# Performance work log

Measured on AMD Instinct MI355X. Metric: run time of the kernel, lower is better.

## Reference

```python
import jax, jax.numpy as jnp
import numpy as np

LAMBDA = 0.7
K = 3
HIDDEN = 8
IN_F = 512
OUT_F = 256
N = 4096


def _gat_layer(x, adj, W, a):
    # h = fc(x); e[i,j] = attn([h_i ; h_j]) = h_i @ a[:F] + h_j @ a[F:]
    # (same math as the N*N repeat/cat/linear, without materializing [N*N, 2F])
    h = x @ W                      # [N, F]
    F_ = h.shape[1]
    src = h @ a[:F_]               # [N, 1]
    dst = h @ a[F_:]               # [N, 1]
    e = src + dst.T                # [N, N]
    att = jax.nn.softmax(e, axis=1) * adj
    return jax.nn.elu(att @ h)     # [N, F]


def setup_inputs() -> dict:
    key = jax.random.key(0)
    ks = jax.random.split(key, 8)
    x = jax.random.normal(ks[0], (N, IN_F), dtype=jnp.float32)
    # binarized sparse-ish adjacency stored densely (avg degree ~41)
    adj = (jax.random.uniform(ks[1], (N, N)) < 0.01).astype(jnp.float32)
    W1 = jax.random.normal(ks[2], (IN_F, HIDDEN), dtype=jnp.float32) * (1.0 / np.sqrt(IN_F))
    a1 = jax.random.normal(ks[3], (2 * HIDDEN, 1), dtype=jnp.float32) * (1.0 / np.sqrt(2 * HIDDEN))
    W2 = jax.random.normal(ks[4], (HIDDEN, 1), dtype=jnp.float32) * (1.0 / np.sqrt(HIDDEN))
    a2 = jax.random.normal(ks[5], (2, 1), dtype=jnp.float32)
    W_sgc = jax.random.normal(ks[6], (IN_F * K, OUT_F), dtype=jnp.float32) * (1.0 / np.sqrt(IN_F * K))
    b_sgc = jnp.zeros((OUT_F,), dtype=jnp.float32)
    return {"x": x, "adj": adj, "W1": W1, "a1": a1, "W2": W2, "a2": a2,
            "W_sgc": W_sgc, "b_sgc": b_sgc}


def reference(x, adj, W1, a1, W2, a2, W_sgc, b_sgc):
    # GAT scoring head (dropout p=0.6 is identity at inference)
    h1 = _gat_layer(x, adj, W1, a1)
    node_scores = _gat_layer(h1, adj, W2, a2)        # [N, 1]

    # K-hop adjacency powers
    adj_list = [adj]
    for _ in range(1, K):
        adj_list.append(adj_list[-1] @ adj)

    # dynamic per-row masking (row-broadcast of node_scores > lambda)
    change_mask = (node_scores > LAMBDA).astype(adj.dtype)  # [N, 1] broadcasts over cols
    for k in range(K - 1):
        adj_list[k] = adj_list[k] * change_mask
        adj_list[k + 1] = adj_list[k + 1] * (1.0 - change_mask)

    # SGC: concat K hop-aggregated features, then linear
    agg = jnp.concatenate([A @ x for A in adj_list], axis=1)  # [N, K*IN_F]
    return agg @ W_sgc + b_sgc
```

## Files before the change

kernel.cpp:

```cpp
#include <hip/hip_runtime.h>
#include <hip/hip_bf16.h>
#include <cstddef>

#define NNODE 4096
#define INF   512
#define OUTF  256
#define HID   8
#define CAP   128

typedef __attribute__((ext_vector_type(8))) short short8;
typedef __attribute__((ext_vector_type(4))) float f32x4;
typedef __attribute__((ext_vector_type(2))) float f32x2;

__device__ __forceinline__ unsigned short f2bf(float f){
  unsigned int u = __float_as_uint(f);
  u += 0x7fffu + ((u >> 16) & 1u);
  return (unsigned short)(u >> 16);
}

__global__ __launch_bounds__(256) void build_csr(const float* __restrict__ adj,
                                                 int* __restrict__ deg,
                                                 int* __restrict__ cols){
  int row = blockIdx.x, tid = threadIdx.x;
  __shared__ int cnt;
  if (tid == 0) cnt = 0;
  __syncthreads();
  const float4* arow = (const float4*)(adj + (size_t)row * NNODE);
  int* crow = cols + (size_t)row * CAP;
  #pragma unroll
  for (int k = 0; k < 4; k++){
    int idx = k * 256 + tid;
    float4 v = arow[idx];
    int n0 = (v.x != 0.f), n1 = (v.y != 0.f), n2 = (v.z != 0.f), n3 = (v.w != 0.f);
    int m = n0 + n1 + n2 + n3;
    if (m){
      int base = atomicAdd(&cnt, m);
      int c = idx * 4;
      if (n0){ if (base < CAP) crow[base] = c;     base++; }
      if (n1){ if (base < CAP) crow[base] = c + 1; base++; }
      if (n2){ if (base < CAP) crow[base] = c + 2; base++; }
      if (n3){ if (base < CAP) crow[base] = c + 3; }
    }
  }
  __syncthreads();
  if (tid == 0) deg[row] = cnt > CAP ? CAP : cnt;
}

__global__ __launch_bounds__(256) void gat_h(const float* __restrict__ x,
                                             const float* __restrict__ W1,
                                             const float* __restrict__ a1,
                                             float* __restrict__ h,
                                             float* __restrict__ dstv,
                                             unsigned short* __restrict__ xb){
  int wave = threadIdx.x >> 6, lane = threadIdx.x & 63;
  int row = blockIdx.x * 4 + wave;
  const float* xr = x + (size_t)row * INF;
  unsigned short* xbr = xb + (size_t)row * INF;
  float acc[HID];
  #pragma unroll
  for (int f = 0; f < HID; f++) acc[f] = 0.f;
  for (int k = lane; k < INF; k += 64){
    float xv = xr[k];
    xbr[k] = f2bf(xv);
    const float* wp = W1 + (size_t)k * HID;
    #pragma unroll
    for (int f = 0; f < HID; f++) acc[f] += xv * wp[f];
  }
  #pragma unroll
  for (int f = 0; f < HID; f++)
    for (int o = 32; o >= 1; o >>= 1) acc[f] += __shfl_xor(acc[f], o, 64);
  if (lane == 0){
    float d = 0.f;
    #pragma unroll
    for (int f = 0; f < HID; f++){ h[(size_t)row*HID + f] = acc[f]; d += acc[f] * a1[HID + f]; }
    dstv[row] = d;
  }
}

__global__ __launch_bounds__(1024) void softmax_p(const float* __restrict__ dstv,
                                                  float* __restrict__ p){
  __shared__ float red[16];
  int tid = threadIdx.x, lane = tid & 63, wv = tid >> 6;
  float mx = -INFINITY;
  for (int i = tid; i < NNODE; i += 1024) mx = fmaxf(mx, dstv[i]);
  #pragma unroll
  for (int o = 32; o >= 1; o >>= 1) mx = fmaxf(mx, __shfl_xor(mx, o, 64));
  if (lane == 0) red[wv] = mx;
  __syncthreads();
  mx = red[0];
  #pragma unroll
  for (int k = 1; k < 16; k++) mx = fmaxf(mx, red[k]);
  __syncthreads();
  float sum = 0.f;
  for (int i = tid; i < NNODE; i += 1024){ float e = expf(dstv[i] - mx); p[i] = e; sum += e; }
  #pragma unroll
  for (int o = 32; o >= 1; o >>= 1) sum += __shfl_xor(sum, o, 64);
  if (lane == 0) red[wv] = sum;
  __syncthreads();
  float tot = 0.f;
  #pragma unroll
  for (int k = 0; k < 16; k++) tot += red[k];
  float inv = 1.0f / tot;
  for (int i = tid; i < NNODE; i += 1024) p[i] *= inv;
}

__global__ __launch_bounds__(256) void gat_agg1(const float* __restrict__ h,
                                                const float* __restrict__ p,
                                                const int* __restrict__ deg,
                                                const int* __restrict__ cols,
                                                const float* __restrict__ W2,
                                                float* __restrict__ h2){
  int wave = threadIdx.x >> 6, lane = threadIdx.x & 63;
  int row = blockIdx.x * 4 + wave;
  const int* cl = cols + (size_t)row * CAP;
  int d = deg[row];
  int ng = lane >> 3;
  int f  = lane & 7;
  float acc = 0.f;
  for (int n = ng; n < d; n += 8){
    int j = cl[n];
    acc += p[j] * h[(size_t)j * HID + f];
  }
  acc += __shfl_xor(acc, 8, 64);
  acc += __shfl_xor(acc, 16, 64);
  acc += __shfl_xor(acc, 32, 64);
  float e = acc > 0.f ? acc : expm1f(acc);
  float t = e * W2[f];
  t += __shfl_xor(t, 1, 64);
  t += __shfl_xor(t, 2, 64);
  t += __shfl_xor(t, 4, 64);
  if (lane == 0) h2[row] = t;
}

__global__ __launch_bounds__(1024) void softmax_q(const float* __restrict__ h2,
                                                  const float* __restrict__ a2,
                                                  float* __restrict__ q){
  __shared__ float red[16];
  int tid = threadIdx.x, lane = tid & 63, wv = tid >> 6;
  float s2 = a2[1];
  float mx = -INFINITY;
  for (int i = tid; i < NNODE; i += 1024) mx = fmaxf(mx, s2 * h2[i]);
  #pragma unroll
  for (int o = 32; o >= 1; o >>= 1) mx = fmaxf(mx, __shfl_xor(mx, o, 64));
  if (lane == 0) red[wv] = mx;
  __syncthreads();
  mx = red[0];
  #pragma unroll
  for (int k = 1; k < 16; k++) mx = fmaxf(mx, red[k]);
  __syncthreads();
  float sum = 0.f;
  for (int i = tid; i < NNODE; i += 1024){ float e = expf(s2 * h2[i] - mx); q[i] = e; sum += e; }
  #pragma unroll
  for (int o = 32; o >= 1; o >>= 1) sum += __shfl_xor(sum, o, 64);
  if (lane == 0) red[wv] = sum;
  __syncthreads();
  float tot = 0.f;
  #pragma unroll
  for (int k = 0; k < 16; k++) tot += red[k];
  float inv = 1.0f / tot;
  for (int i = tid; i < NNODE; i += 1024) q[i] = q[i] * inv * h2[i];
}

__global__ __launch_bounds__(256) void scores_mask(const float* __restrict__ q,
                                                   const int* __restrict__ deg,
                                                   const int* __restrict__ cols,
                                                   float* __restrict__ maskf){
  int wave = threadIdx.x >> 6, lane = threadIdx.x & 63;
  int row = blockIdx.x * 4 + wave;
  const int* cl = cols + (size_t)row * CAP;
  int d = deg[row];
  float s = 0.f;
  for (int n = lane; n < d; n += 64) s += q[cl[n]];
  #pragma unroll
  for (int o = 32; o >= 1; o >>= 1) s += __shfl_xor(s, o, 64);
  if (lane == 0){
    float e = s > 0.f ? s : expm1f(s);
    maskf[row] = (e > 0.7f) ? 1.0f : 0.0f;
  }
}

__global__ void convert_w(const float* __restrict__ Wsgc, unsigned short* __restrict__ wbT){
  int idx = blockIdx.x * 256 + threadIdx.x;
  if (idx >= 512 * 512) return;
  int c = idx >> 9, k = idx & 511;
  float val = (c < 256) ? Wsgc[(size_t)k * OUTF + c]
                        : Wsgc[(size_t)(1024 + k) * OUTF + (c - 256)];
  wbT[idx] = f2bf(val);
}

__global__ __launch_bounds__(256) void gemm_xw(const unsigned short* __restrict__ XB,
                                               const unsigned short* __restrict__ BT,
                                               float* __restrict__ G){
  __shared__ unsigned short As[64][72];
  __shared__ unsigned short Bs[64][72];
  int tid = threadIdx.x;
  int wave = tid >> 6, lane = tid & 63;
  int row0 = blockIdx.x * 64;
  int col0 = blockIdx.y * 64;
  int wr = wave >> 1, wc = wave & 1;
  f32x4 acc[2][2];
  #pragma unroll
  for (int i = 0; i < 2; i++)
    #pragma unroll
    for (int j = 0; j < 2; j++)
      #pragma unroll
      for (int e = 0; e < 4; e++) acc[i][j][e] = 0.f;

  int mrow = lane & 15;
  int kq = (lane >> 4) * 8;

  for (int k0 = 0; k0 < 512; k0 += 64){
    #pragma unroll
    for (int ps = 0; ps < 2; ps++){
      int idx = ps * 256 + tid;
      int r = idx >> 3;
      int ko = (idx & 7) * 8;
      *(int4*)(&As[r][ko]) = *(const int4*)(XB + ((size_t)(row0 + r) * 512 + k0 + ko));
      *(int4*)(&Bs[r][ko]) = *(const int4*)(BT + ((size_t)(col0 + r) * 512 + k0 + ko));
    }
    __syncthreads();
    #pragma unroll
    for (int kk = 0; kk < 2; kk++){
      short8 a[2], b[2];
      #pragma unroll
      for (int i = 0; i < 2; i++)
        a[i] = *(const short8*)(&As[wr * 32 + i * 16 + mrow][kk * 32 + kq]);
      #pragma unroll
      for (int j = 0; j < 2; j++)
        b[j] = *(const short8*)(&Bs[wc * 32 + j * 16 + mrow][kk * 32 + kq]);
      #pragma unroll
      for (int i = 0; i < 2; i++)
        #pragma unroll
        for (int j = 0; j < 2; j++)
          acc[i][j] = __builtin_amdgcn_mfma_f32_16x16x32_bf16(a[i], b[j], acc[i][j], 0, 0, 0);
    }
    __syncthreads();
  }
  int crow = (lane >> 4) * 4;
  int ccol = lane & 15;
  #pragma unroll
  for (int i = 0; i < 2; i++)
    #pragma unroll
    for (int j = 0; j < 2; j++)
      #pragma unroll
      for (int e = 0; e < 4; e++){
        int r = row0 + wr * 32 + i * 16 + crow + e;
        int c = col0 + wc * 32 + j * 16 + ccol;
        G[(size_t)r * 512 + c] = acc[i][j][e];
      }
}

__global__ __launch_bounds__(256) void hop_half(const float* __restrict__ in, int instride,
                                                int colbase,
                                                float* __restrict__ out,
                                                const int* __restrict__ deg,
                                                const int* __restrict__ cols){
  int wave = threadIdx.x >> 6, lane = threadIdx.x & 63;
  int row = blockIdx.x * 4 + wave;
  const int* cl = cols + (size_t)row * CAP;
  int d = deg[row];
  const float* src = in + colbase;
  f32x2 acc = {0.f, 0.f};
  f32x2 acc2 = {0.f, 0.f};
  int n = 0;
  for (; n + 8 <= d; n += 8){
    int j0 = cl[n],   j1 = cl[n+1], j2 = cl[n+2], j3 = cl[n+3];
    int j4 = cl[n+4], j5 = cl[n+5], j6 = cl[n+6], j7 = cl[n+7];
    f32x2 a = ((const f32x2*)(src + (size_t)j0 * instride))[lane];
    f32x2 b = ((const f32x2*)(src + (size_t)j1 * instride))[lane];
    f32x2 c = ((const f32x2*)(src + (size_t)j2 * instride))[lane];
    f32x2 e = ((const f32x2*)(src + (size_t)j3 * instride))[lane];
    f32x2 f = ((const f32x2*)(src + (size_t)j4 * instride))[lane];
    f32x2 g = ((const f32x2*)(src + (size_t)j5 * instride))[lane];
    f32x2 hh = ((const f32x2*)(src + (size_t)j6 * instride))[lane];
    f32x2 ii = ((const f32x2*)(src + (size_t)j7 * instride))[lane];
    acc  += a + b + c + e;
    acc2 += f + g + hh + ii;
  }
  for (; n < d; n++)
    acc += ((const f32x2*)(src + (size_t)cl[n] * instride))[lane];
  ((f32x2*)(out + (size_t)row * OUTF + colbase))[lane] = acc + acc2;
}

__global__ __launch_bounds__(256) void hop_final_half(const float* __restrict__ Gleft,
                                                      const float* __restrict__ T2,
                                                      const float* __restrict__ maskf,
                                                      const float* __restrict__ b,
                                                      int colbase,
                                                      float* __restrict__ out,
                                                      const int* __restrict__ deg,
                                                      const int* __restrict__ cols){
  int wave = threadIdx.x >> 6, lane = threadIdx.x & 63;
  int row = blockIdx.x * 4 + wave;
  const int* cl = cols + (size_t)row * CAP;
  int d = deg[row];
  bool m = maskf[row] != 0.0f;
  const float* src = (m ? Gleft : T2) + colbase;
  int instride    = m ? 512   : 256;
  f32x2 acc = {0.f, 0.f};
  f32x2 acc2 = {0.f, 0.f};
  int n = 0;
  for (; n + 8 <= d; n += 8){
    int j0 = cl[n],   j1 = cl[n+1], j2 = cl[n+2], j3 = cl[n+3];
    int j4 = cl[n+4], j5 = cl[n+5], j6 = cl[n+6], j7 = cl[n+7];
    f32x2 a = ((const f32x2*)(src + (size_t)j0 * instride))[lane];
    f32x2 bb = ((const f32x2*)(src + (size_t)j1 * instride))[lane];
    f32x2 c = ((const f32x2*)(src + (size_t)j2 * instride))[lane];
    f32x2 e = ((const f32x2*)(src + (size_t)j3 * instride))[lane];
    f32x2 f = ((const f32x2*)(src + (size_t)j4 * instride))[lane];
    f32x2 g = ((const f32x2*)(src + (size_t)j5 * instride))[lane];
    f32x2 hh = ((const f32x2*)(src + (size_t)j6 * instride))[lane];
    f32x2 ii = ((const f32x2*)(src + (size_t)j7 * instride))[lane];
    acc  += a + bb + c + e;
    acc2 += f + g + hh + ii;
  }
  for (; n < d; n++)
    acc += ((const f32x2*)(src + (size_t)cl[n] * instride))[lane];
  f32x2 bias = ((const f32x2*)(b + colbase))[lane];
  ((f32x2*)(out + (size_t)row * OUTF + colbase))[lane] = acc + acc2 + bias;
}

extern "C" void kernel_launch(void* const* d_in, const int* in_sizes, int n_in,
                              void* d_out, int out_size, void* d_ws, size_t ws_size,
                              hipStream_t stream) {
  const float* x    = (const float*)d_in[0];
  const float* adj  = (const float*)d_in[1];
  const float* W1   = (const float*)d_in[2];
  const float* a1   = (const float*)d_in[3];
  const float* W2   = (const float*)d_in[4];
  const float* a2   = (const float*)d_in[5];
  const float* Wsgc = (const float*)d_in[6];
  const float* bsgc = (const float*)d_in[7];
  float* out = (float*)d_out;

  char* w = (char*)d_ws;
  size_t off = 0;
  auto carve = [&](size_t bytes) -> char* {
    char* p = w + off;
    off += (bytes + 255) & ~(size_t)255;
    return p;
  };
  int*   deg   = (int*)carve((size_t)NNODE * 4);
  int*   cols  = (int*)carve((size_t)NNODE * CAP * 4);
  float* h     = (float*)carve((size_t)NNODE * HID * 4);
  float* dstv  = (float*)carve((size_t)NNODE * 4);
  float* p     = (float*)carve((size_t)NNODE * 4);
  float* h2    = (float*)carve((size_t)NNODE * 4);
  float* q     = (float*)carve((size_t)NNODE * 4);
  float* maskf = (float*)carve((size_t)NNODE * 4);
  unsigned short* wbT = (unsigned short*)carve((size_t)512 * 512 * 2);
  unsigned short* xb  = (unsigned short*)carve((size_t)NNODE * INF * 2);
  float* G  = (float*)carve((size_t)NNODE * 512 * 4);
  float* T1 = (float*)carve((size_t)NNODE * OUTF * 4);
  float* T2 = (float*)carve((size_t)NNODE * OUTF * 4);

  build_csr<<<NNODE, 256, 0, stream>>>(adj, deg, cols);

  gat_h<<<NNODE / 4, 256, 0, stream>>>(x, W1, a1, h, dstv, xb);
  softmax_p<<<1, 1024, 0, stream>>>(dstv, p);
  gat_agg1<<<NNODE / 4, 256, 0, stream>>>(h, p, deg, cols, W2, h2);
  softmax_q<<<1, 1024, 0, stream>>>(h2, a2, q);
  scores_mask<<<NNODE / 4, 256, 0, stream>>>(q, deg, cols, maskf);

  convert_w<<<1024, 256, 0, stream>>>(Wsgc, wbT);
  dim3 gg(64, 8);
  gemm_xw<<<gg, 256, 0, stream>>>(xb, wbT, G);

  hop_half<<<NNODE / 4, 256, 0, stream>>>(G + 256, 512, 0,   T1, deg, cols);
  hop_half<<<NNODE / 4, 256, 0, stream>>>(G + 256, 512, 128, T1, deg, cols);
  hop_half<<<NNODE / 4, 256, 0, stream>>>(T1, 256, 0,   T2, deg, cols);
  hop_half<<<NNODE / 4, 256, 0, stream>>>(T1, 256, 128, T2, deg, cols);
  hop_final_half<<<NNODE / 4, 256, 0, stream>>>(G, T2, maskf, bsgc, 0,   out, deg, cols);
  hop_final_half<<<NNODE / 4, 256, 0, stream>>>(G, T2, maskf, bsgc, 128, out, deg, cols);
}
```

Before: 205.6 us.

## Store hop intermediates in bf16, pad CSR rows, merge hop halves, enlarge GEMM tile

The GEMM output G and the hop buffers T1/T2 are now stored as bf16 instead of fp32, which halves the bytes moved by the sparse gather kernels. CSR rows are padded to a multiple of 8 with a sentinel index that points at a zeroed extra row, so the tail handling is simpler. Each hop now runs as one kernel where half-waves gather 8 bf16 values per lane and combine with a shuffle, and the GEMM tile grows from 64x64 to 128x128. The cost is extra rounding error from bf16 intermediates and higher register pressure in the GEMM.

```diff
diff --git a/kernel.cpp b/kernel.cpp
--- a/kernel.cpp
+++ b/kernel.cpp
@@ -10,12 +10,14 @@
 
 typedef __attribute__((ext_vector_type(8))) short short8;
 typedef __attribute__((ext_vector_type(4))) float f32x4;
-typedef __attribute__((ext_vector_type(2))) float f32x2;
 
 __device__ __forceinline__ unsigned short f2bf(float f){
   unsigned int u = __float_as_uint(f);
   u += 0x7fffu + ((u >> 16) & 1u);
   return (unsigned short)(u >> 16);
+}
+__device__ __forceinline__ float bf2f(unsigned short s){
+  return __uint_as_float((unsigned int)s << 16);
 }
 
 __global__ __launch_bounds__(256) void build_csr(const float* __restrict__ adj,
@@ -43,7 +45,11 @@
     }
   }
   __syncthreads();
-  if (tid == 0) deg[row] = cnt > CAP ? CAP : cnt;
+  int c = cnt > CAP ? CAP : cnt;
+  int c8 = (c + 7) & ~7;
+  if (c8 > CAP) c8 = CAP;
+  if (tid < c8 - c) crow[c + tid] = NNODE;
+  if (tid == 0) deg[row] = c8;
 }
 
 __global__ __launch_bounds__(256) void gat_h(const float* __restrict__ x,
@@ -52,6 +58,8 @@
                                              float* __restrict__ h,
                                              float* __restrict__ dstv,
                                              unsigned short* __restrict__ xb){
+  if (blockIdx.x == 0 && threadIdx.x < HID)
+    h[(size_t)NNODE * HID + threadIdx.x] = 0.f;
   int wave = threadIdx.x >> 6, lane = threadIdx.x & 63;
   int row = blockIdx.x * 4 + wave;
   const float* xr = x + (size_t)row * INF;
@@ -81,6 +89,7 @@
                                                   float* __restrict__ p){
   __shared__ float red[16];
   int tid = threadIdx.x, lane = tid & 63, wv = tid >> 6;
+  if (tid == 0) p[NNODE] = 0.f;
   float mx = -INFINITY;
   for (int i = tid; i < NNODE; i += 1024) mx = fmaxf(mx, dstv[i]);
   #pragma unroll
@@ -137,6 +146,7 @@
                                                   float* __restrict__ q){
   __shared__ float red[16];
   int tid = threadIdx.x, lane = tid & 63, wv = tid >> 6;
+  if (tid == 0) q[NNODE] = 0.f;
   float s2 = a2[1];
   float mx = -INFINITY;
   for (int i = tid; i < NNODE; i += 1024) mx = fmaxf(mx, s2 * h2[i]);
@@ -179,8 +189,13 @@
   }
 }
 
-__global__ void convert_w(const float* __restrict__ Wsgc, unsigned short* __restrict__ wbT){
+__global__ void convert_w(const float* __restrict__ Wsgc, unsigned short* __restrict__ wbT,
+                          unsigned short* __restrict__ Gb,
+                          unsigned short* __restrict__ T1,
+                          unsigned short* __restrict__ T2){
   int idx = blockIdx.x * 256 + threadIdx.x;
+  if (idx < 512) Gb[(size_t)NNODE * 512 + idx] = 0;
+  if (idx < 256){ T1[(size_t)NNODE * 256 + idx] = 0; T2[(size_t)NNODE * 256 + idx] = 0; }
   if (idx >= 512 * 512) return;
   int c = idx >> 9, k = idx & 511;
   float val = (c < 256) ? Wsgc[(size_t)k * OUTF + c]
@@ -190,19 +205,19 @@
 
 __global__ __launch_bounds__(256) void gemm_xw(const unsigned short* __restrict__ XB,
                                                const unsigned short* __restrict__ BT,
-                                               float* __restrict__ G){
-  __shared__ unsigned short As[64][72];
-  __shared__ unsigned short Bs[64][72];
+                                               unsigned short* __restrict__ Gb){
+  __shared__ unsigned short As[128][72];
+  __shared__ unsigned short Bs[128][72];
   int tid = threadIdx.x;
   int wave = tid >> 6, lane = tid & 63;
-  int row0 = blockIdx.x * 64;
-  int col0 = blockIdx.y * 64;
+  int row0 = blockIdx.x * 128;
+  int col0 = blockIdx.y * 128;
   int wr = wave >> 1, wc = wave & 1;
-  f32x4 acc[2][2];
-  #pragma unroll
-  for (int i = 0; i < 2; i++)
-    #pragma unroll
-    for (int j = 0; j < 2; j++)
+  f32x4 acc[4][4];
+  #pragma unroll
+  for (int i = 0; i < 4; i++)
+    #pragma unroll
+    for (int j = 0; j < 4; j++)
       #pragma unroll
       for (int e = 0; e < 4; e++) acc[i][j][e] = 0.f;
 
@@ -211,7 +226,7 @@
 
   for (int k0 = 0; k0 < 512; k0 += 64){
     #pragma unroll
-    for (int ps = 0; ps < 2; ps++){
+    for (int ps = 0; ps < 4; ps++){
       int idx = ps * 256 + tid;
       int r = idx >> 3;
       int ko = (idx & 7) * 8;
@@ -221,17 +236,17 @@
     __syncthreads();
     #pragma unroll
     for (int kk = 0; kk < 2; kk++){
-      short8 a[2], b[2];
+      short8 a[4], b[4];
       #pragma unroll
-      for (int i = 0; i < 2; i++)
-        a[i] = *(const short8*)(&As[wr * 32 + i * 16 + mrow][kk * 32 + kq]);
+      for (int i = 0; i < 4; i++)
+        a[i] = *(const short8*)(&As[wr * 64 + i * 16 + mrow][kk * 32 + kq]);
       #pragma unroll
-      for (int j = 0; j < 2; j++)
-        b[j] = *(const short8*)(&Bs[wc * 32 + j * 16 + mrow][kk * 32 + kq]);
+      for (int j = 0; j < 4; j++)
+        b[j] = *(const short8*)(&Bs[wc * 64 + j * 16 + mrow][kk * 32 + kq]);
       #pragma unroll
-      for (int i = 0; i < 2; i++)
+      for (int i = 0; i < 4; i++)
         #pragma unroll
-        for (int j = 0; j < 2; j++)
+        for (int j = 0; j < 4; j++)
           acc[i][j] = __builtin_amdgcn_mfma_f32_16x16x32_bf16(a[i], b[j], acc[i][j], 0, 0, 0);
     }
     __syncthreads();
@@ -239,85 +254,136 @@
   int crow = (lane >> 4) * 4;
   int ccol = lane & 15;
   #pragma unroll
-  for (int i = 0; i < 2; i++)
-    #pragma unroll
-    for (int j = 0; j < 2; j++)
+  for (int i = 0; i < 4; i++)
+    #pragma unroll
+    for (int j = 0; j < 4; j++)
       #pragma unroll
       for (int e = 0; e < 4; e++){
-        int r = row0 + wr * 32 + i * 16 + crow + e;
-        int c = col0 + wc * 32 + j * 16 + ccol;
-        G[(size_t)r * 512 + c] = acc[i][j][e];
+        int r = row0 + wr * 64 + i * 16 + crow + e;
+        int c = col0 + wc * 64 + j * 16 + ccol;
+        Gb[(size_t)r * 512 + c] = f2bf(acc[i][j][e]);
       }
 }
 
-__global__ __launch_bounds__(256) void hop_half(const float* __restrict__ in, int instride,
-                                                int colbase,
-                                                float* __restrict__ out,
-                                                const int* __restrict__ deg,
-                                                const int* __restrict__ cols){
+__global__ __launch_bounds__(256) void hop_bf(const unsigned short* __restrict__ in, int instride,
+                                              int colbase,
+                                              unsigned short* __restrict__ out,
+                                              const int* __restrict__ deg,
+                                              const int* __restrict__ cols){
   int wave = threadIdx.x >> 6, lane = threadIdx.x & 63;
   int row = blockIdx.x * 4 + wave;
   const int* cl = cols + (size_t)row * CAP;
   int d = deg[row];
-  const float* src = in + colbase;
-  f32x2 acc = {0.f, 0.f};
-  f32x2 acc2 = {0.f, 0.f};
+  int half = lane >> 5, cid = lane & 31;
+  const unsigned short* src = in + colbase + cid * 8;
+  float acc[8];
+  #pragma unroll
+  for (int e = 0; e < 8; e++) acc[e] = 0.f;
   int n = 0;
-  for (; n + 8 <= d; n += 8){
-    int j0 = cl[n],   j1 = cl[n+1], j2 = cl[n+2], j3 = cl[n+3];
-    int j4 = cl[n+4], j5 = cl[n+5], j6 = cl[n+6], j7 = cl[n+7];
-    f32x2 a = ((const f32x2*)(src + (size_t)j0 * instride))[lane];
-    f32x2 b = ((const f32x2*)(src + (size_t)j1 * instride))[lane];
-    f32x2 c = ((const f32x2*)(src + (size_t)j2 * instride))[lane];
-    f32x2 e = ((const f32x2*)(src + (size_t)j3 * instride))[lane];
-    f32x2 f = ((const f32x2*)(src + (size_t)j4 * instride))[lane];
-    f32x2 g = ((const f32x2*)(src + (size_t)j5 * instride))[lane];
-    f32x2 hh = ((const f32x2*)(src + (size_t)j6 * instride))[lane];
-    f32x2 ii = ((const f32x2*)(src + (size_t)j7 * instride))[lane];
-    acc  += a + b + c + e;
-    acc2 += f + g + hh + ii;
-  }
-  for (; n < d; n++)
-    acc += ((const f32x2*)(src + (size_t)cl[n] * instride))[lane];
-  ((f32x2*)(out + (size_t)row * OUTF + colbase))[lane] = acc + acc2;
-}
-
-__global__ __launch_bounds__(256) void hop_final_half(const float* __restrict__ Gleft,
-                                                      const float* __restrict__ T2,
-                                                      const float* __restrict__ maskf,
-                                                      const float* __restrict__ b,
-                                                      int colbase,
-                                                      float* __restrict__ out,
-                                                      const int* __restrict__ deg,
-                                                      const int* __restrict__ cols){
+  for (; n + 16 <= d; n += 16){
+    int j0 = cl[n +      half], j1 = cl[n + 2  + half], j2 = cl[n + 4  + half], j3 = cl[n + 6  + half];
+    int j4 = cl[n + 8  + half], j5 = cl[n + 10 + half], j6 = cl[n + 12 + half], j7 = cl[n + 14 + half];
+    short8 v0 = *(const short8*)(src + (size_t)j0 * instride);
+    short8 v1 = *(const short8*)(src + (size_t)j1 * instride);
+    short8 v2 = *(const short8*)(src + (size_t)j2 * instride);
+    short8 v3 = *(const short8*)(src + (size_t)j3 * instride);
+    short8 v4 = *(const short8*)(src + (size_t)j4 * instride);
+    short8 v5 = *(const short8*)(src + (size_t)j5 * instride);
+    short8 v6 = *(const short8*)(src + (size_t)j6 * instride);
+    short8 v7 = *(const short8*)(src + (size_t)j7 * instride);
+    #pragma unroll
+    for (int e = 0; e < 8; e++){
+      acc[e] += bf2f((unsigned short)v0[e]) + bf2f((unsigned short)v1[e])
+              + bf2f((unsigned short)v2[e]) + bf2f((unsigned short)v3[e])
+              + bf2f((unsigned short)v4[e]) + bf2f((unsigned short)v5[e])
+              + bf2f((unsigned short)v6[e]) + bf2f((unsigned short)v7[e]);
+    }
+  }
+  if (n < d){
+    int j0 = cl[n + half], j1 = cl[n + 2 + half], j2 = cl[n + 4 + half], j3 = cl[n + 6 + half];
+    short8 v0 = *(const short8*)(src + (size_t)j0 * instride);
+    short8 v1 = *(const short8*)(src + (size_t)j1 * instride);
+    short8 v2 = *(const short8*)(src + (size_t)j2 * instride);
+    short8 v3 = *(const short8*)(src + (size_t)j3 * instride);
+    #pragma unroll
+    for (int e = 0; e < 8; e++){
+      acc[e] += bf2f((unsigned short)v0[e]) + bf2f((unsigned short)v1[e])
+              + bf2f((unsigned short)v2[e]) + bf2f((unsigned short)v3[e]);
+    }
+  }
+  #pragma unroll
+  for (int e = 0; e < 8; e++) acc[e] += __shfl_xor(acc[e], 32, 64);
+  if (half == 0){
+    union { short8 v; unsigned short u[8]; } pk;
+    #pragma unroll
+    for (int e = 0; e < 8; e++) pk.u[e] = f2bf(acc[e]);
+    *(short8*)(out + (size_t)row * OUTF + cid * 8) = pk.v;
+  }
+}
+
+__global__ __launch_bounds__(256) void hop_final_bf(const unsigned short* __restrict__ Gb,
+                                                    const unsigned short* __restrict__ T2,
+                                                    const float* __restrict__ maskf,
+                                                    const float* __restrict__ b,
+                                                    float* __restrict__ out,
+                                                    const int* __restrict__ deg,
+                                                    const int* __restrict__ cols){
   int wave = threadIdx.x >> 6, lane = threadIdx.x & 63;
   int row = blockIdx.x * 4 + wave;
   const int* cl = cols + (size_t)row * CAP;
   int d = deg[row];
   bool m = maskf[row] != 0.0f;
-  const float* src = (m ? Gleft : T2) + colbase;
-  int instride    = m ? 512   : 256;
-  f32x2 acc = {0.f, 0.f};
-  f32x2 acc2 = {0.f, 0.f};
+  const unsigned short* base = m ? Gb : T2;
+  int instride = m ? 512 : 256;
+  int half = lane >> 5, cid = lane & 31;
+  const unsigned short* src = base + cid * 8;
+  float acc[8];
+  #pragma unroll
+  for (int e = 0; e < 8; e++) acc[e] = 0.f;
   int n = 0;
-  for (; n + 8 <= d; n += 8){
-    int j0 = cl[n],   j1 = cl[n+1], j2 = cl[n+2], j3 = cl[n+3];
-    int j4 = cl[n+4], j5 = cl[n+5], j6 = cl[n+6], j7 = cl[n+7];
-    f32x2 a = ((const f32x2*)(src + (size_t)j0 * instride))[lane];
-    f32x2 bb = ((const f32x2*)(src + (size_t)j1 * instride))[lane];
-    f32x2 c = ((const f32x2*)(src + (size_t)j2 * instride))[lane];
-    f32x2 e = ((const f32x2*)(src + (size_t)j3 * instride))[lane];
-    f32x2 f = ((const f32x2*)(src + (size_t)j4 * instride))[lane];
-    f32x2 g = ((const f32x2*)(src + (size_t)j5 * instride))[lane];
-    f32x2 hh = ((const f32x2*)(src + (size_t)j6 * instride))[lane];
-    f32x2 ii = ((const f32x2*)(src + (size_t)j7 * instride))[lane];
-    acc  += a + bb + c + e;
-    acc2 += f + g + hh + ii;
-  }
-  for (; n < d; n++)
-    acc += ((const f32x2*)(src + (size_t)cl[n] * instride))[lane];
-  f32x2 bias = ((const f32x2*)(b + colbase))[lane];
-  ((f32x2*)(out + (size_t)row * OUTF + colbase))[lane] = acc + acc2 + bias;
+  for (; n + 16 <= d; n += 16){
+    int j0 = cl[n +      half], j1 = cl[n + 2  + half], j2 = cl[n + 4  + half], j3 = cl[n + 6  + half];
+    int j4 = cl[n + 8  + half], j5 = cl[n + 10 + half], j6 = cl[n + 12 + half], j7 = cl[n + 14 + half];
+    short8 v0 = *(const short8*)(src + (size_t)j0 * instride);
+    short8 v1 = *(const short8*)(src + (size_t)j1 * instride);
+    short8 v2 = *(const short8*)(src + (size_t)j2 * instride);
+    short8 v3 = *(const short8*)(src + (size_t)j3 * instride);
+    short8 v4 = *(const short8*)(src + (size_t)j4 * instride);
+    short8 v5 = *(const short8*)(src + (size_t)j5 * instride);
+    short8 v6 = *(const short8*)(src + (size_t)j6 * instride);
+    short8 v7 = *(const short8*)(src + (size_t)j7 * instride);
+    #pragma unroll
+    for (int e = 0; e < 8; e++){
+      acc[e] += bf2f((unsigned short)v0[e]) + bf2f((unsigned short)v1[e])
+              + bf2f((unsigned short)v2[e]) + bf2f((unsigned short)v3[e])
+              + bf2f((unsigned short)v4[e]) + bf2f((unsigned short)v5[e])
+              + bf2f((unsigned short)v6[e]) + bf2f((unsigned short)v7[e]);
+    }
+  }
+  if (n < d){
+    int j0 = cl[n + half], j1 = cl[n + 2 + half], j2 = cl[n + 4 + half], j3 = cl[n + 6 + half];
+    short8 v0 = *(const short8*)(src + (size_t)j0 * instride);
+    short8 v1 = *(const short8*)(src + (size_t)j1 * instride);
+    short8 v2 = *(const short8*)(src + (size_t)j2 * instride);
+    short8 v3 = *(const short8*)(src + (size_t)j3 * instride);
+    #pragma unroll
+    for (int e = 0; e < 8; e++){
+      acc[e] += bf2f((unsigned short)v0[e]) + bf2f((unsigned short)v1[e])
+              + bf2f((unsigned short)v2[e]) + bf2f((unsigned short)v3[e]);
+    }
+  }
+  #pragma unroll
+  for (int e = 0; e < 8; e++) acc[e] += __shfl_xor(acc[e], 32, 64);
+  if (half == 0){
+    f32x4 b0 = ((const f32x4*)(b + cid * 8))[0];
+    f32x4 b1 = ((const f32x4*)(b + cid * 8 + 4))[0];
+    f32x4 o0, o1;
+    #pragma unroll
+    for (int e = 0; e < 4; e++){ o0[e] = acc[e] + b0[e]; o1[e] = acc[4 + e] + b1[e]; }
+    float* orow = out + (size_t)row * OUTF + cid * 8;
+    ((f32x4*)orow)[0] = o0;
+    ((f32x4*)(orow + 4))[0] = o1;
+  }
 }
 
 extern "C" void kernel_launch(void* const* d_in, const int* in_sizes, int n_in,
@@ -342,17 +408,17 @@
   };
   int*   deg   = (int*)carve((size_t)NNODE * 4);
   int*   cols  = (int*)carve((size_t)NNODE * CAP * 4);
-  float* h     = (float*)carve((size_t)NNODE * HID * 4);
+  float* h     = (float*)carve((size_t)(NNODE + 1) * HID * 4);
   float* dstv  = (float*)carve((size_t)NNODE * 4);
-  float* p     = (float*)carve((size_t)NNODE * 4);
+  float* p     = (float*)carve((size_t)(NNODE + 1) * 4);
   float* h2    = (float*)carve((size_t)NNODE * 4);
-  float* q     = (float*)carve((size_t)NNODE * 4);
+  float* q     = (float*)carve((size_t)(NNODE + 1) * 4);
   float* maskf = (float*)carve((size_t)NNODE * 4);
   unsigned short* wbT = (unsigned short*)carve((size_t)512 * 512 * 2);
   unsigned short* xb  = (unsigned short*)carve((size_t)NNODE * INF * 2);
-  float* G  = (float*)carve((size_t)NNODE * 512 * 4);
-  float* T1 = (float*)carve((size_t)NNODE * OUTF * 4);
-  float* T2 = (float*)carve((size_t)NNODE * OUTF * 4);
+  unsigned short* Gb  = (unsigned short*)carve((size_t)(NNODE + 1) * 512 * 2);
+  unsigned short* T1  = (unsigned short*)carve((size_t)(NNODE + 1) * OUTF * 2);
+  unsigned short* T2  = (unsigned short*)carve((size_t)(NNODE + 1) * OUTF * 2);
 
   build_csr<<<NNODE, 256, 0, stream>>>(adj, deg, cols);
 
@@ -362,14 +428,11 @@
   softmax_q<<<1, 1024, 0, stream>>>(h2, a2, q);
   scores_mask<<<NNODE / 4, 256, 0, stream>>>(q, deg, cols, maskf);
 
-  convert_w<<<1024, 256, 0, stream>>>(Wsgc, wbT);
-  dim3 gg(64, 8);
-  gemm_xw<<<gg, 256, 0, stream>>>(xb, wbT, G);
-
-  hop_half<<<NNODE / 4, 256, 0, stream>>>(G + 256, 512, 0,   T1, deg, cols);
-  hop_half<<<NNODE / 4, 256, 0, stream>>>(G + 256, 512, 128, T1, deg, cols);
-  hop_half<<<NNODE / 4, 256, 0, stream>>>(T1, 256, 0,   T2, deg, cols);
-  hop_half<<<NNODE / 4, 256, 0, stream>>>(T1, 256, 128, T2, deg, cols);
-  hop_final_half<<<NNODE / 4, 256, 0, stream>>>(G, T2, maskf, bsgc, 0,   out, deg, cols);
-  hop_final_half<<<NNODE / 4, 256, 0, stream>>>(G, T2, maskf, bsgc, 128, out, deg, cols);
-}
+  convert_w<<<1024, 256, 0, stream>>>(Wsgc, wbT, Gb, T1, T2);
+  dim3 gg(32, 4);
+  gemm_xw<<<gg, 256, 0, stream>>>(xb, wbT, Gb);
+
+  hop_bf<<<NNODE / 4, 256, 0, stream>>>(Gb, 512, 256, T1, deg, cols);
+  hop_bf<<<NNODE / 4, 256, 0, stream>>>(T1, 256, 0,  T2, deg, cols);
+  hop_final_bf<<<NNODE / 4, 256, 0, stream>>>(Gb, T2, maskf, bsgc, out, deg, cols);
+}
```

Result: faster. 172.6 us (-16.0%).
